# Performance work log

Measured on AMD Instinct MI355X. Metric: run time of the kernel, lower is better.

The kernel has to match this reference:

```python
import jax, jax.numpy as jnp
import numpy as np
from jax import lax

SPARSITY = 0.5  # args.sparsity: fraction of weights KEPT


def get_subnet(scores, k):
    """GetSubnet.forward: sort |scores|, zero lowest (1-k) fraction, one elsewhere."""
    sa = jnp.abs(scores)
    n = sa.size
    j = int((1.0 - k) * n)  # static: number of entries zeroed
    idx = jnp.argsort(sa.ravel())  # ascending, matches torch .sort()
    mask = jnp.zeros((n,), dtype=sa.dtype).at[idx[j:]].set(1.0)
    return mask.reshape(scores.shape)


def masked_conv(x, w, s, b, stride):
    m = get_subnet(s, SPARSITY)
    y = lax.conv_general_dilated(
        x, w * m, window_strides=(stride, stride), padding=((1, 1), (1, 1)),
        dimension_numbers=('NCHW', 'OIHW', 'NCHW'))
    return y + b[None, :, None, None]


def setup_inputs() -> dict:
    key = jax.random.key(0)
    ks = jax.random.split(key, 16)
    def rn(k, shape, scale):
        return jax.random.normal(k, shape, dtype=jnp.float32) * scale
    return {
        'x':   rn(ks[0], (64, 3, 64, 64), 1.0),
        'w1':  rn(ks[1], (128, 3, 3, 3), 0.2),   's1': rn(ks[2], (128, 3, 3, 3), 1.0),   'b1': rn(ks[3], (128,), 0.01),
        'w2':  rn(ks[4], (256, 128, 3, 3), 0.05), 's2': rn(ks[5], (256, 128, 3, 3), 1.0), 'b2': rn(ks[6], (256,), 0.01),
        'w3':  rn(ks[7], (512, 256, 3, 3), 0.03), 's3': rn(ks[8], (512, 256, 3, 3), 1.0), 'b3': rn(ks[9], (512,), 0.01),
        'fw1': rn(ks[10], (1024, 512), 0.05),     'fs1': rn(ks[11], (1024, 512), 1.0),    'fb1': rn(ks[12], (1024,), 0.01),
        'fw2': rn(ks[13], (10, 1024), 0.05),      'fs2': rn(ks[14], (10, 1024), 1.0),     'fb2': rn(ks[15], (10,), 0.01),
    }


def reference(x, w1, s1, b1, w2, s2, b2, w3, s3, b3, fw1, fs1, fb1, fw2, fs2, fb2):
    h = jax.nn.relu(masked_conv(x, w1, s1, b1, stride=1))   # [64,128,64,64]
    h = jax.nn.relu(masked_conv(h, w2, s2, b2, stride=2))   # [64,256,32,32]
    h = jax.nn.relu(masked_conv(h, w3, s3, b3, stride=2))   # [64,512,16,16]
    h = h.mean(axis=(2, 3))                                 # [64,512] global avg pool
    m1 = get_subnet(fs1, SPARSITY)
    h = jax.nn.relu(h @ (fw1 * m1).T + fb1)                 # [64,1024]
    m2 = get_subnet(fs2, SPARSITY)
    return h @ (fw2 * m2).T + fb2                           # [64,10]
```

## Files before the change

kernel.cpp:

```cpp
#include <hip/hip_runtime.h>
#include <stdint.h>


typedef __attribute__((ext_vector_type(8))) short short8;
typedef __attribute__((ext_vector_type(4))) short short4v;
typedef __attribute__((ext_vector_type(4))) float floatx4;

__device__ __forceinline__ unsigned short f2bf(float f) {
    unsigned u = __float_as_uint(f);
    u += 0x7fffu + ((u >> 16) & 1u);
    return (unsigned short)(u >> 16);
}

constexpr unsigned CUM0 = 3456u;
constexpr unsigned CUM1 = 298368u;
constexpr unsigned CUM2 = 1478016u;
constexpr unsigned CUM3 = 2002304u;
constexpr unsigned STOT = 2012544u;
constexpr int NBH = 512;

__device__ __forceinline__ int find_tensor(unsigned idx, unsigned& li) {
    if (idx < CUM0) { li = idx;        return 0; }
    if (idx < CUM1) { li = idx - CUM0; return 1; }
    if (idx < CUM2) { li = idx - CUM1; return 2; }
    if (idx < CUM3) { li = idx - CUM2; return 3; }
    li = idx - CUM3; return 4;
}

__global__ __launch_bounds__(256) void hist11(const float* __restrict__ s0,
                                              const float* __restrict__ s1,
                                              const float* __restrict__ s2,
                                              const float* __restrict__ s3,
                                              const float* __restrict__ s4,
                                              const unsigned* __restrict__ P,
                                              unsigned* __restrict__ ghist, int pass) {
    __shared__ unsigned lh[10240];
    const int tid = threadIdx.x;
    const int NB = (pass == 2) ? 512 : 2048;
    for (int i = tid; i < NB * 5; i += 256) lh[i] = 0;
    __syncthreads();

    unsigned pref[5];
    #pragma unroll
    for (int t = 0; t < 5; t++) pref[t] = pass ? P[t] : 0u;
    const int fsh = (pass == 1) ? 20 : 9;

    for (unsigned idx = blockIdx.x * 256u + tid; idx < STOT; idx += NBH * 256u) {
        unsigned li; int t = find_tensor(idx, li);
        const float* sp = t == 0 ? s0 : t == 1 ? s1 : t == 2 ? s2 : t == 3 ? s3 : s4;
        unsigned key = __float_as_uint(sp[li]) & 0x7fffffffu;
        bool ok = (pass == 0) || ((key >> fsh) == pref[t]);
        if (ok) {
            unsigned bin = (pass == 0) ? (key >> 20)
                         : (pass == 1) ? ((key >> 9) & 2047u)
                                       : (key & 511u);
            atomicAdd(&lh[(unsigned)t * NB + bin], 1u);
        }
    }
    __syncthreads();
    const int goff = (pass == 0) ? 0 : (pass == 1) ? 10240 : 20480;
    for (int i = tid; i < NB * 5; i += 256) {
        unsigned v = lh[i];
        if (v) atomicAdd(&ghist[goff + i], v);
    }
}

__global__ __launch_bounds__(256) void find11(const unsigned* __restrict__ ghist,
                                              unsigned* __restrict__ P,
                                              unsigned* __restrict__ targ, int pass) {
    const int t = blockIdx.x;
    const int tid = threadIdx.x;
    const int NB = (pass == 2) ? 512 : 2048;
    const int goff = (pass == 0) ? 0 : (pass == 1) ? 10240 : 20480;
    const int seg = NB / 256;
    __shared__ unsigned bins[2048];
    __shared__ unsigned part[256];
    for (int i = tid; i < NB; i += 256) bins[i] = ghist[goff + t * NB + i];
    __syncthreads();
    unsigned s = 0;
    for (int j = 0; j < seg; j++) s += bins[tid * seg + j];
    part[tid] = s;
    __syncthreads();
    if (tid == 0) {
        unsigned n = t == 0 ? 3456u : t == 1 ? 294912u : t == 2 ? 1179648u
                   : t == 3 ? 524288u : 10240u;
        unsigned target = (pass == 0) ? (n >> 1) : targ[t];
        unsigned cum = 0; int q = 0;
        for (; q < 256; q++) { unsigned c = part[q]; if (cum + c > target) break; cum += c; }
        int b = q * seg;
        for (;; b++) { unsigned c = bins[b]; if (cum + c > target) break; cum += c; }
        targ[t] = target - cum;
        if (pass == 0)      P[t] = (unsigned)b;
        else if (pass == 1) P[t] = (P[t] << 11) | (unsigned)b;
        else                P[t] = (P[t] << 9) | (unsigned)b;
    }
}

__global__ void mask_reorder(const float* __restrict__ w0, const float* __restrict__ w1,
                             const float* __restrict__ w2, const float* __restrict__ w3,
                             const float* __restrict__ w4,
                             const float* __restrict__ s0, const float* __restrict__ s1,
                             const float* __restrict__ s2, const float* __restrict__ s3,
                             const float* __restrict__ s4,
                             const unsigned* __restrict__ T,
                             float* __restrict__ wm1,
                             unsigned short* __restrict__ A2,
                             unsigned short* __restrict__ A3,
                             float* __restrict__ fwm1, float* __restrict__ fwm2,
                             float* __restrict__ pooled) {
    unsigned idx = blockIdx.x * 256u + threadIdx.x;
    if (idx >= STOT) return;
    if (idx < 32768u) pooled[idx] = 0.f;
    unsigned li; int t = find_tensor(idx, li);
    const float* sp = t == 0 ? s0 : t == 1 ? s1 : t == 2 ? s2 : t == 3 ? s3 : s4;
    const float* wp = t == 0 ? w0 : t == 1 ? w1 : t == 2 ? w2 : t == 3 ? w3 : w4;
    unsigned key = __float_as_uint(sp[li]) & 0x7fffffffu;
    float val = (key >= T[t]) ? wp[li] : 0.f;
    if (t == 0) {
        wm1[li] = val;
    } else if (t == 1) {
        unsigned k = li / 1152u, r = li - k * 1152u;
        unsigned c = r / 9u, e = r - c * 9u;
        A2[((size_t)e * 256u + k) * 128u + c] = f2bf(val);
    } else if (t == 2) {
        unsigned k = li / 2304u, r = li - k * 2304u;
        unsigned c = r / 9u, e = r - c * 9u;
        A3[((size_t)e * 512u + k) * 256u + c] = f2bf(val);
    } else if (t == 3) {
        fwm1[li] = val;
    } else {
        fwm2[li] = val;
    }
}

template <int C, int H, int W, int K, int TX, int TY, int KT>
__global__ __launch_bounds__(TX* TY) void conv_direct(const float* __restrict__ in,
                                                      const float* __restrict__ wm,
                                                      const float* __restrict__ bias,
                                                      unsigned short* __restrict__ out) {
    constexpr int TILW = TX * 2, TILH = TY * 2;
    constexpr int ITW = TILW + 2, ITH = TILH + 2;
    constexpr int NTHREADS = TX * TY;
    constexpr int NLOAD = (ITH * ITW + NTHREADS - 1) / NTHREADS;
    constexpr int KG = K / KT;

    __shared__ float sIn[ITH * ITW];
    __shared__ float sW[9 * KT];

    const int tid = threadIdx.x;
    const int tx = tid % TX, ty = tid / TX;
    const int kg = blockIdx.z % KG, n = blockIdx.z / KG;
    const int ox0 = blockIdx.x * TILW, oy0 = blockIdx.y * TILH;
    const int ix0 = ox0 - 1, iy0 = oy0 - 1;

    const float* inN = in + (size_t)n * C * H * W;
    const float* wkg = wm + (size_t)kg * KT * C * 9;

    int goff[NLOAD];
    #pragma unroll
    for (int i = 0; i < NLOAD; i++) {
        int idx = tid + i * NTHREADS;
        if (idx < ITH * ITW) {
            int r = idx / ITW, col = idx % ITW;
            int gy = iy0 + r, gx = ix0 + col;
            goff[i] = (gy >= 0 && gy < H && gx >= 0 && gx < W) ? (gy * W + gx) : -1;
        } else goff[i] = -2;
    }

    float acc[2][2][KT];
    #pragma unroll
    for (int py = 0; py < 2; py++)
        #pragma unroll
        for (int px = 0; px < 2; px++)
            #pragma unroll
            for (int j = 0; j < KT; j++) acc[py][px][j] = 0.f;

    for (int c = 0; c < C; c++) {
        const float* inC = inN + (size_t)c * H * W;
        #pragma unroll
        for (int i = 0; i < NLOAD; i++) {
            int g = goff[i];
            if (g >= -1) sIn[tid + i * NTHREADS] = (g >= 0) ? inC[g] : 0.f;
        }
        for (int i = tid; i < 9 * KT; i += NTHREADS) {
            int e = i / KT, j = i % KT;
            sW[i] = wkg[j * C * 9 + c * 9 + e];
        }
        __syncthreads();

        float vin[4][4];
        const float* base = &sIn[(ty * 2) * ITW + tx * 2];
        #pragma unroll
        for (int r = 0; r < 4; r++)
            #pragma unroll
            for (int cc = 0; cc < 4; cc++) vin[r][cc] = base[r * ITW + cc];

        #pragma unroll
        for (int e = 0; e < 9; e++) {
            const int dy = e / 3, dx = e % 3;
            #pragma unroll
            for (int j = 0; j < KT; j++) {
                float wv = sW[e * KT + j];
                #pragma unroll
                for (int py = 0; py < 2; py++)
                    #pragma unroll
                    for (int px = 0; px < 2; px++)
                        acc[py][px][j] = fmaf(vin[py + dy][px + dx], wv, acc[py][px][j]);
            }
        }
        __syncthreads();
    }

    float bj[KT];
    #pragma unroll
    for (int j = 0; j < KT; j++) bj[j] = bias[kg * KT + j];
    #pragma unroll
    for (int py = 0; py < 2; py++)
        #pragma unroll
        for (int px = 0; px < 2; px++) {
            int oy = oy0 + ty * 2 + py, ox = ox0 + tx * 2 + px;
            short8 v;
            #pragma unroll
            for (int j = 0; j < KT; j++) {
                float t = acc[py][px][j] + bj[j];
                v[j] = (short)f2bf(t > 0.f ? t : 0.f);
            }
            *(short8*)(out + ((size_t)(n * H + oy) * W + ox) * K + kg * KT) = v;
        }
}

template <int C, int H, int W, int KOUT, int NPIX, bool POOL, bool SWAPYZ>
__global__ __launch_bounds__(256, 4) void conv_mfma(const unsigned short* __restrict__ in,
                                                    const unsigned short* __restrict__ A,
                                                    const float* __restrict__ bias,
                                                    void* __restrict__ outv) {
    constexpr int OH = H / 2, OW = W / 2;
    constexpr int PR = NPIX / OW;
    constexpr int FN = NPIX / 16;
    constexpr int RH = 2 * PR + 1;
    constexpr int IW = W + 1;
    constexpr int NC = C / 32;
    constexpr int PSTR = 40;
    constexpr int NSLOT = RH * IW * 4;
    constexpr int SLMAX = (NSLOT + 255) / 256;

    __shared__ unsigned short sIn[RH * IW * PSTR];

    const int tid = threadIdx.x;
    const int lane = tid & 63;
    const int wv = tid >> 6;
    const int l15 = lane & 15;
    const int quad = lane >> 4;
    const int pt = blockIdx.x;
    const int kb = SWAPYZ ? blockIdx.z : blockIdx.y;
    const int n  = SWAPYZ ? blockIdx.y : blockIdx.z;
    const int k0 = kb * 128;
    const int oy0 = pt * PR;
    const int g0y = 2 * oy0 - 1;
    const int mw = wv * 32;

    int goff[SLMAX], slds[SLMAX];
    #pragma unroll
    for (int i = 0; i < SLMAX; i++) {
        int s = tid + i * 256;
        if (s < NSLOT) {
            int q = s & 3, pix = s >> 2;
            int ix = pix % IW, iy = pix / IW;
            int gy = g0y + iy, gx = ix - 1;
            slds[i] = pix * PSTR + q * 8;
            goff[i] = (gy >= 0 && gy < H && gx >= 0) ? ((gy * W + gx) * C + q * 8) : -1;
        } else { goff[i] = -2; slds[i] = 0; }
    }

    int pB[FN];
    #pragma unroll
    for (int fn = 0; fn < FN; fn++) {
        int p = fn * 16 + l15;
        int oyl = p / OW, oxl = p % OW;
        pB[fn] = (oyl * 2 * IW + oxl * 2) * PSTR + quad * 8;
    }

    const unsigned short* inN = in + (size_t)n * H * W * C;

    floatx4 acc[2][FN];
    #pragma unroll
    for (int fm = 0; fm < 2; fm++)
        #pragma unroll
        for (int fn = 0; fn < FN; fn++) acc[fm][fn] = (floatx4){0.f, 0.f, 0.f, 0.f};

    #pragma unroll 1
    for (int cc = 0; cc < NC; cc++) {
        const int cof = cc * 32;
        const unsigned short* Abase = A + (size_t)(k0 + mw + l15) * C + cof + quad * 8;
        const size_t estr = (size_t)KOUT * C;

        __syncthreads();

        short8 af[9][2];
        short8 bf[9][FN];

        af[0][0] = *(const short8*)(Abase);
        af[0][1] = *(const short8*)(Abase + 16 * C);
        af[1][0] = *(const short8*)(Abase + estr);
        af[1][1] = *(const short8*)(Abase + estr + 16 * C);

        #pragma unroll
        for (int i = 0; i < SLMAX; i++) {
            int g = goff[i];
            if (g >= 0) {
                *(short8*)&sIn[slds[i]] = *(const short8*)(inN + g + cof);
            } else if (g == -1 && cc == 0) {
                *(short8*)&sIn[slds[i]] = (short8){0, 0, 0, 0, 0, 0, 0, 0};
            }
        }
        __syncthreads();

        #pragma unroll
        for (int fn = 0; fn < FN; fn++)
            bf[0][fn] = *(const short8*)&sIn[pB[fn]];

        #pragma unroll
        for (int e = 0; e < 9; e++) {
            if (e + 2 < 9) {
                af[e + 2][0] = *(const short8*)(Abase + (size_t)(e + 2) * estr);
                af[e + 2][1] = *(const short8*)(Abase + (size_t)(e + 2) * estr + 16 * C);
            }
            if (e + 1 < 9) {
                const int dy1 = (e + 1) / 3, dx1 = (e + 1) - dy1 * 3;
                const int boff = (dy1 * IW + dx1) * PSTR;
                #pragma unroll
                for (int fn = 0; fn < FN; fn++)
                    bf[e + 1][fn] = *(const short8*)&sIn[pB[fn] + boff];
            }
            #pragma unroll
            for (int fn = 0; fn < FN; fn++) {
                acc[0][fn] = __builtin_amdgcn_mfma_f32_16x16x32_bf16(af[e][0], bf[e][fn], acc[0][fn], 0, 0, 0);
                acc[1][fn] = __builtin_amdgcn_mfma_f32_16x16x32_bf16(af[e][1], bf[e][fn], acc[1][fn], 0, 0, 0);
            }
        }
    }

    if (!POOL) {
        unsigned short* out = (unsigned short*)outv;
        #pragma unroll
        for (int fm = 0; fm < 2; fm++) {
            const int k4 = k0 + mw + fm * 16 + quad * 4;
            float b0 = bias[k4], b1 = bias[k4 + 1], b2 = bias[k4 + 2], b3 = bias[k4 + 3];
            #pragma unroll
            for (int fn = 0; fn < FN; fn++) {
                int p = fn * 16 + l15;
                int oy = oy0 + p / OW, ox = p % OW;
                float v0 = acc[fm][fn][0] + b0, v1 = acc[fm][fn][1] + b1;
                float v2 = acc[fm][fn][2] + b2, v3 = acc[fm][fn][3] + b3;
                short4v v;
                v[0] = (short)f2bf(v0 > 0.f ? v0 : 0.f);
                v[1] = (short)f2bf(v1 > 0.f ? v1 : 0.f);
                v[2] = (short)f2bf(v2 > 0.f ? v2 : 0.f);
                v[3] = (short)f2bf(v3 > 0.f ? v3 : 0.f);
                *(short4v*)(out + ((size_t)(n * OH + oy) * OW + ox) * KOUT + k4) = v;
            }
        }
    } else {
        float* out = (float*)outv;
        #pragma unroll
        for (int fm = 0; fm < 2; fm++) {
            #pragma unroll
            for (int reg = 0; reg < 4; reg++) {
                int k = k0 + mw + fm * 16 + quad * 4 + reg;
                float bv = bias[k];
                float s = 0.f;
                #pragma unroll
                for (int fn = 0; fn < FN; fn++) {
                    float v = acc[fm][fn][reg] + bv;
                    s += v > 0.f ? v : 0.f;
                }
                s += __shfl_xor(s, 1); s += __shfl_xor(s, 2);
                s += __shfl_xor(s, 4); s += __shfl_xor(s, 8);
                if (l15 == 0) atomicAdd(&out[n * KOUT + k], s * (1.0f / (OH * OW)));
            }
        }
    }
}

__global__ void fc1_kernel(const float* __restrict__ pooled, const float* __restrict__ w,
                           const float* __restrict__ b, float* __restrict__ out) {
    int t = blockIdx.x * 256 + threadIdx.x;
    int o = t & 1023, n = t >> 10;
    const float4* w4 = (const float4*)(w + (size_t)o * 512);
    const float4* p4 = (const float4*)(pooled + (size_t)n * 512);
    float acc = 0.f;
    for (int i = 0; i < 128; i++) {
        float4 a = p4[i], ww = w4[i];
        acc += a.x * ww.x + a.y * ww.y + a.z * ww.z + a.w * ww.w;
    }
    acc += b[o];
    out[t] = acc > 0.f ? acc : 0.f;
}

__global__ void fc2_kernel(const float* __restrict__ h, const float* __restrict__ w,
                           const float* __restrict__ b, float* __restrict__ out) {
    int n = blockIdx.x, tid = threadIdx.x;
    __shared__ float redw[40];
    const float4* h4 = (const float4*)(h + (size_t)n * 1024);
    float4 a = h4[tid];
    for (int o = 0; o < 10; o++) {
        const float4* w4 = (const float4*)(w + (size_t)o * 1024);
        float4 ww = w4[tid];
        float v = a.x * ww.x + a.y * ww.y + a.z * ww.z + a.w * ww.w;
        for (int off = 32; off > 0; off >>= 1) v += __shfl_down(v, off);
        if ((tid & 63) == 0) redw[o * 4 + (tid >> 6)] = v;
    }
    __syncthreads();
    if (tid < 10) {
        float s = redw[tid * 4] + redw[tid * 4 + 1] + redw[tid * 4 + 2] + redw[tid * 4 + 3] + b[tid];
        out[n * 10 + tid] = s;
    }
}

extern "C" void kernel_launch(void* const* d_in, const int* in_sizes, int n_in,
                              void* d_out, int out_size, void* d_ws, size_t ws_size,
                              hipStream_t stream) {
    const float* x   = (const float*)d_in[0];
    const float* w1  = (const float*)d_in[1];
    const float* s1  = (const float*)d_in[2];
    const float* b1  = (const float*)d_in[3];
    const float* w2  = (const float*)d_in[4];
    const float* s2  = (const float*)d_in[5];
    const float* b2  = (const float*)d_in[6];
    const float* w3  = (const float*)d_in[7];
    const float* s3  = (const float*)d_in[8];
    const float* b3  = (const float*)d_in[9];
    const float* fw1 = (const float*)d_in[10];
    const float* fs1 = (const float*)d_in[11];
    const float* fb1 = (const float*)d_in[12];
    const float* fw2 = (const float*)d_in[13];
    const float* fs2 = (const float*)d_in[14];
    const float* fb2 = (const float*)d_in[15];
    float* out = (float*)d_out;

    char* ws = (char*)d_ws;
    size_t off = 0;
    auto alloc = [&](size_t bytes) -> char* {
        char* p = ws + off;
        off = (off + bytes + 255) & ~(size_t)255;
        return p;
    };
    unsigned* ghist = (unsigned*)alloc(23040ull * 4);
    unsigned* P     = (unsigned*)alloc(64);
    unsigned* targ  = (unsigned*)alloc(64);
    float* wm1  = (float*)alloc(3456ull * 4);
    float* fwm1 = (float*)alloc(524288ull * 4);
    float* fwm2 = (float*)alloc(10240ull * 4);
    unsigned short* A2 = (unsigned short*)alloc(294912ull * 2);
    unsigned short* A3 = (unsigned short*)alloc(1179648ull * 2);
    unsigned short* h1 = (unsigned short*)alloc(33554432ull * 2);
    unsigned short* h2 = (unsigned short*)alloc(16777216ull * 2);
    float* pooled = (float*)alloc(32768ull * 4);
    float* fc1h   = (float*)alloc(65536ull * 4);
    if (off > ws_size) return;

    (void)hipMemsetAsync(ghist, 0, 23040ull * 4, stream);

    for (int pass = 0; pass < 3; pass++) {
        hist11<<<NBH, 256, 0, stream>>>(s1, s2, s3, fs1, fs2, P, ghist, pass);
        find11<<<5, 256, 0, stream>>>(ghist, P, targ, pass);
    }
    int gs = (STOT + 255) / 256;
    mask_reorder<<<gs, 256, 0, stream>>>(w1, w2, w3, fw1, fw2, s1, s2, s3, fs1, fs2, P,
                                         wm1, A2, A3, fwm1, fwm2, pooled);

    conv_direct<3, 64, 64, 128, 16, 16, 8>
        <<<dim3(2, 2, 64 * 16), 256, 0, stream>>>(x, wm1, b1, h1);
    conv_mfma<128, 64, 64, 256, 64, false, false>
        <<<dim3(16, 2, 64), 256, 0, stream>>>(h1, A2, b2, h2);
    conv_mfma<256, 32, 32, 512, 64, true, true>
        <<<dim3(4, 64, 4), 256, 0, stream>>>(h2, A3, b3, pooled);

    fc1_kernel<<<256, 256, 0, stream>>>(pooled, fwm1, fb1, fc1h);
    fc2_kernel<<<64, 256, 0, stream>>>(fc1h, fwm2, fb2, out);
}
```

Measured before the change: 420.0 us.

## Issue all weight fragment loads before LDS staging and lower occupancy bound

```diff
diff --git a/kernel.cpp b/kernel.cpp
--- a/kernel.cpp
+++ b/kernel.cpp
@@ -5,11 +5,20 @@
 typedef __attribute__((ext_vector_type(8))) short short8;
 typedef __attribute__((ext_vector_type(4))) short short4v;
 typedef __attribute__((ext_vector_type(4))) float floatx4;
+typedef __attribute__((ext_vector_type(4))) int int4v;
 
 __device__ __forceinline__ unsigned short f2bf(float f) {
     unsigned u = __float_as_uint(f);
     u += 0x7fffu + ((u >> 16) & 1u);
     return (unsigned short)(u >> 16);
+}
+
+__device__ __forceinline__ short8 gload16(const unsigned short* p) {
+    int4v d;
+    asm volatile("global_load_dwordx4 %0, %1, off" : "=v"(d) : "v"(p));
+    union { int4v i; short8 s; } u;
+    u.i = d;
+    return u.s;
 }
 
 constexpr unsigned CUM0 = 3456u;
@@ -230,7 +239,7 @@
 }
 
 template <int C, int H, int W, int KOUT, int NPIX, bool POOL, bool SWAPYZ>
-__global__ __launch_bounds__(256, 4) void conv_mfma(const unsigned short* __restrict__ in,
+__global__ __launch_bounds__(256, 3) void conv_mfma(const unsigned short* __restrict__ in,
                                                     const unsigned short* __restrict__ A,
                                                     const float* __restrict__ bias,
                                                     void* __restrict__ outv) {
@@ -297,12 +306,11 @@
         __syncthreads();
 
         short8 af[9][2];
-        short8 bf[9][FN];
-
-        af[0][0] = *(const short8*)(Abase);
-        af[0][1] = *(const short8*)(Abase + 16 * C);
-        af[1][0] = *(const short8*)(Abase + estr);
-        af[1][1] = *(const short8*)(Abase + estr + 16 * C);
+        #pragma unroll
+        for (int e = 0; e < 9; e++) {
+            af[e][0] = gload16(Abase + (size_t)e * estr);
+            af[e][1] = gload16(Abase + (size_t)e * estr + 16 * C);
+        }
 
         #pragma unroll
         for (int i = 0; i < SLMAX; i++) {
@@ -314,28 +322,21 @@
             }
         }
         __syncthreads();
-
-        #pragma unroll
-        for (int fn = 0; fn < FN; fn++)
-            bf[0][fn] = *(const short8*)&sIn[pB[fn]];
+        asm volatile("s_waitcnt vmcnt(0)" ::: "memory");
+        __builtin_amdgcn_sched_barrier(0);
 
         #pragma unroll
         for (int e = 0; e < 9; e++) {
-            if (e + 2 < 9) {
-                af[e + 2][0] = *(const short8*)(Abase + (size_t)(e + 2) * estr);
-                af[e + 2][1] = *(const short8*)(Abase + (size_t)(e + 2) * estr + 16 * C);
-            }
-            if (e + 1 < 9) {
-                const int dy1 = (e + 1) / 3, dx1 = (e + 1) - dy1 * 3;
-                const int boff = (dy1 * IW + dx1) * PSTR;
-                #pragma unroll
-                for (int fn = 0; fn < FN; fn++)
-                    bf[e + 1][fn] = *(const short8*)&sIn[pB[fn] + boff];
-            }
+            const int dy = e / 3, dx = e - dy * 3;
+            const int boff = (dy * IW + dx) * PSTR;
+            short8 bfr[FN];
+            #pragma unroll
+            for (int fn = 0; fn < FN; fn++)
+                bfr[fn] = *(const short8*)&sIn[pB[fn] + boff];
             #pragma unroll
             for (int fn = 0; fn < FN; fn++) {
-                acc[0][fn] = __builtin_amdgcn_mfma_f32_16x16x32_bf16(af[e][0], bf[e][fn], acc[0][fn], 0, 0, 0);
-                acc[1][fn] = __builtin_amdgcn_mfma_f32_16x16x32_bf16(af[e][1], bf[e][fn], acc[1][fn], 0, 0, 0);
+                acc[0][fn] = __builtin_amdgcn_mfma_f32_16x16x32_bf16(af[e][0], bfr[fn], acc[0][fn], 0, 0, 0);
+                acc[1][fn] = __builtin_amdgcn_mfma_f32_16x16x32_bf16(af[e][1], bfr[fn], acc[1][fn], 0, 0, 0);
             }
         }
     }
```

New measurement: 459.0 us. +9.3%, slower.
